# Performance work log

Hardware: AMD Instinct MI355X
Metric: run time of the kernel (lower is better)

Reference implementation:

```python
import jax, jax.numpy as jnp
import numpy as np

B, R, T, N = 64, 2, 32, 128
C_IN, C_OUT = 64, 64
PRELU_INIT = 0.25


def setup_inputs() -> dict:
    key = jax.random.key(0)
    ks = jax.random.split(key, 6)
    x = jax.random.normal(ks[0], (B, C_IN, T, N), dtype=jnp.float32)
    A = jax.random.uniform(ks[1], (B, R, T, N, N), dtype=jnp.float32)  # non-negative adjacency
    # per-relation 1x1 conv (t_kernel_size=1, relation=1 per gcn since split=[])
    w_gcn = jax.random.normal(ks[2], (R, C_OUT, C_IN), dtype=jnp.float32) * (1.0 / np.sqrt(C_IN))
    b_gcn = jnp.zeros((R, C_OUT), dtype=jnp.float32)
    # tcn temporal conv: kernel (3,1), padding (1,0)
    w_tcn = jax.random.normal(ks[3], (C_OUT, C_OUT, 3, 1), dtype=jnp.float32) * (1.0 / np.sqrt(3 * C_OUT))
    b_tcn = jnp.zeros((C_OUT,), dtype=jnp.float32)
    a_tcn = jnp.float32(PRELU_INIT)  # PReLU inside tcn
    a_out = jnp.float32(PRELU_INIT)  # final PReLU
    return {"x": x, "A": A, "w_gcn": w_gcn, "b_gcn": b_gcn,
            "w_tcn": w_tcn, "b_tcn": b_tcn, "a_tcn": a_tcn, "a_out": a_out}


def _prelu(x, a):
    return jnp.where(x >= 0, x, a * x)


def _normalized_laplacian_tilde(A):
    # A: (..., N, N); A_tilde = A + I, return D^{-1/2} A_tilde D^{-1/2}
    n = A.shape[-1]
    A_t = A + jnp.eye(n, dtype=A.dtype)
    d_inv_sqrt = jax.lax.rsqrt(A_t.sum(-1))  # (..., N); rowsum >= 1
    return d_inv_sqrt[..., :, None] * A_t * d_inv_sqrt[..., None, :]


def reference(x, A, w_gcn, b_gcn, w_tcn, b_tcn, a_tcn, a_out):
    # x: (B,C,T,N), A: (B,R,T,N,N). Eval mode: drop_edge is identity, dropout inactive.
    res = x  # in_channels == out_channels, stride == 1
    # per-relation 1x1 convs, batched over R
    x_c = jnp.einsum('bctn,roc->brotn', x, w_gcn) + b_gcn[None, :, :, None, None]
    A_norm = _normalized_laplacian_tilde(A)  # (B,R,T,N,N)
    # bmm per (r,t): out[b,c,m] = sum_n x_c[b,r,c,t,n] * A_norm[b,r,t,n,m], summed over r
    x_comb = jnp.einsum('brctn,brtnm->bctm', x_c, A_norm)
    # tcn: PReLU -> Conv2d (3,1) pad (1,0) -> Dropout(0)
    h = _prelu(x_comb, a_tcn)
    h = jax.lax.conv_general_dilated(
        h, w_tcn, window_strides=(1, 1), padding=((1, 1), (0, 0)),
        dimension_numbers=('NCHW', 'OIHW', 'NCHW'))
    h = h + b_tcn[None, :, None, None]
    out = _prelu(h + res, a_out)
    return (out, A)
```

## Files before the change

kernel.cpp:

```cpp
#include <hip/hip_runtime.h>
#include <hip/hip_bf16.h>

typedef unsigned short u16;
typedef unsigned int u32;
typedef __attribute__((ext_vector_type(8))) short bf16x8;
typedef __attribute__((ext_vector_type(4))) float f32x4;
typedef __attribute__((ext_vector_type(4))) u16 u16x4;
typedef __attribute__((ext_vector_type(8))) u16 u16x8;

#define B_ 64
#define R_ 2
#define T_ 32
#define N_ 128
#define C_ 64

__device__ __forceinline__ u16 f2bf(float f) {
  return __builtin_bit_cast(u16, __float2bfloat16(f));
}
__device__ __forceinline__ float bf2f(u16 h) {
  u32 u = ((u32)h) << 16;
  return __builtin_bit_cast(float, u);
}

#define MFMA __builtin_amdgcn_mfma_f32_16x16x32_bf16

#define BAR()                                                  \
  do {                                                         \
    asm volatile("s_waitcnt lgkmcnt(0)" ::: "memory");         \
    __builtin_amdgcn_s_barrier();                              \
    __builtin_amdgcn_sched_barrier(0);                         \
  } while (0)

__device__ __forceinline__ void a_load(float4* av, const float* Aslice, int ch, int tid) {
  const int arow = tid >> 2, aseg = tid & 3;
  const float* ap = Aslice + (size_t)(ch * 64 + arow) * N_ + aseg * 32;
#pragma unroll
  for (int j = 0; j < 8; ++j) av[j] = *(const float4*)(ap + 4 * j);
}
__device__ __forceinline__ void a_store(const float4* av, float* Oslice, int ch, int tid) {
  const int arow = tid >> 2, aseg = tid & 3;
  float* op = Oslice + (size_t)(ch * 64 + arow) * N_ + aseg * 32;
#pragma unroll
  for (int j = 0; j < 8; ++j) *(float4*)(op + 4 * j) = av[j];
}

__device__ __forceinline__ void at_write(const float4* av, int ch, int tid,
                                         u16 (*AT)[64], float* dinvr) {
  const int arow = tid >> 2, aseg = tid & 3;
  const int n = ch * 64 + arow;
  float part = 0.f;
#pragma unroll
  for (int j = 0; j < 8; ++j) part += (av[j].x + av[j].y) + (av[j].z + av[j].w);
  part += __shfl_xor(part, 1);
  part += __shfl_xor(part, 2);
  const float d = rsqrtf(part + 1.0f);
  if (aseg == 0) dinvr[n] = d;
  const int col = arow ^ (aseg << 4);
#pragma unroll
  for (int j = 0; j < 8; ++j) {
#pragma unroll
    for (int k = 0; k < 4; ++k) {
      const int m = aseg * 32 + 4 * j + k;
      float v = ((const float*)&av[j])[k];
      if (m == n) v += 1.0f;
      AT[m][col] = f2bf(v * d);
    }
  }
}

__device__ __forceinline__ void load_wg(bf16x8 wf[2][2], const float* wg, int r,
                                        int wr, int lr, int lg) {
#pragma unroll
  for (int kk = 0; kk < 2; ++kk)
#pragma unroll
    for (int mr = 0; mr < 2; ++mr) {
      const float* p = wg + ((size_t)(r * C_ + 32 * wr + 16 * mr + lr)) * C_ + 32 * kk + 8 * lg;
      float4 a = *(const float4*)p, b = *(const float4*)(p + 4);
      bf16x8 f;
      f[0] = (short)f2bf(a.x); f[1] = (short)f2bf(a.y);
      f[2] = (short)f2bf(a.z); f[3] = (short)f2bf(a.w);
      f[4] = (short)f2bf(b.x); f[5] = (short)f2bf(b.y);
      f[6] = (short)f2bf(b.z); f[7] = (short)f2bf(b.w);
      wf[kk][mr] = f;
    }
}

__device__ __forceinline__ void mm1f(u16 (*TMP)[128], const bf16x8 wf[2][2],
                                     const bf16x8 bfr[2][4], const float4 bias[2],
                                     int wr, int wc, int lr, int lg) {
  f32x4 acc1[2][4] = {};
#pragma unroll
  for (int kk = 0; kk < 2; ++kk)
#pragma unroll
    for (int mr = 0; mr < 2; ++mr)
#pragma unroll
      for (int nc = 0; nc < 4; ++nc)
        acc1[mr][nc] = MFMA(wf[kk][mr], bfr[kk][nc], acc1[mr][nc], 0, 0, 0);
#pragma unroll
  for (int mr = 0; mr < 2; ++mr) {
    const int o0 = 32 * wr + 16 * mr + 4 * lg;
    const float bb[4] = {bias[mr].x, bias[mr].y, bias[mr].z, bias[mr].w};
#pragma unroll
    for (int nc = 0; nc < 4; ++nc) {
      const int n = 64 * wc + 16 * nc + lr;
#pragma unroll
      for (int i = 0; i < 4; ++i)
        TMP[o0 + i][n ^ (i << 4)] = f2bf(acc1[mr][nc][i] + bb[i]);
    }
  }
}

__device__ __forceinline__ void mm2_half(f32x4 accr[2][4], const u16 (*TMP)[128],
                                         const u16 (*AT)[64], int ch,
                                         int wr, int wc, int lr, int lg) {
#pragma unroll
  for (int kkin = 0; kkin < 2; ++kkin) {
    bf16x8 af[2], bfr[4];
#pragma unroll
    for (int mr = 0; mr < 2; ++mr) {
      const int c = 32 * wr + 16 * mr + lr;
      const int colT = (ch * 64 + 32 * kkin + 8 * lg) ^ ((lr & 3) << 4);
      af[mr] = *(const bf16x8*)&TMP[c][colT];
    }
#pragma unroll
    for (int nc = 0; nc < 4; ++nc) {
      const int m = 64 * wc + 16 * nc + lr;
      const int colA = (32 * kkin + 8 * lg) ^ (((m >> 5) & 3) << 4);
      bfr[nc] = *(const bf16x8*)&AT[m][colA];
    }
#pragma unroll
    for (int mr = 0; mr < 2; ++mr)
#pragma unroll
      for (int nc = 0; nc < 4; ++nc)
        accr[mr][nc] = MFMA(af[mr], bfr[nc], accr[mr][nc], 0, 0, 0);
  }
}

__device__ __forceinline__ void fold(f32x4 acc2[2][4], f32x4 accr[2][4],
                                     const float* dinvr, int wc, int lr) {
#pragma unroll
  for (int nc = 0; nc < 4; ++nc) {
    const float dm = dinvr[64 * wc + 16 * nc + lr];
#pragma unroll
    for (int mr = 0; mr < 2; ++mr)
#pragma unroll
      for (int i = 0; i < 4; ++i) {
        acc2[mr][nc][i] += dm * accr[mr][nc][i];
        accr[mr][nc][i] = 0.f;
      }
  }
}

__global__ __launch_bounds__(256, 2) void k_gcn(
    const float* __restrict__ x, const float* __restrict__ A,
    const float* __restrict__ wg, const float* __restrict__ bg,
    float* __restrict__ outA, u16* __restrict__ wsX) {
  __shared__ __align__(16) u16 AT[2][N_][64];
  __shared__ __align__(16) u16 TMP[C_][128];
  __shared__ float dinv[R_][N_];

  const int tid = threadIdx.x;
  const int bid = ((blockIdx.x & 7) << 8) | (blockIdx.x >> 3);
  const int b = bid >> 5, t = bid & 31;
  const int lane = tid & 63, wv = tid >> 6;
  const int wr = wv >> 1, wc = wv & 1;
  const int lr = lane & 15, lg = lane >> 4;

  const size_t Asl0 = ((size_t)((b * R_ + 0) * T_ + t)) * (size_t)(N_ * N_);
  const size_t Asl1 = ((size_t)((b * R_ + 1) * T_ + t)) * (size_t)(N_ * N_);

  float4 xv[8];
  {
    const int c = tid & 63, ub = tid >> 6;
    const float* xp = x + ((size_t)(b * C_ + c) * T_ + t) * N_ + 32 * ub;
#pragma unroll
    for (int j = 0; j < 8; ++j) xv[j] = *(const float4*)(xp + 4 * j);
  }
  float4 avA[8], avB[8];
  a_load(avA, A + Asl0, 0, tid);
  a_load(avB, A + Asl0, 1, tid);
  bf16x8 wf0[2][2];
  load_wg(wf0, wg, 0, wr, lr, lg);
  float4 bias[R_][2];
#pragma unroll
  for (int r = 0; r < R_; ++r)
#pragma unroll
    for (int mr = 0; mr < 2; ++mr)
      bias[r][mr] = *(const float4*)(bg + r * C_ + 32 * wr + 16 * mr + 4 * lg);

  u16 (*XT)[64] = (u16(*)[64])TMP;
  {
    const int c = tid & 63, ub = tid >> 6;
#pragma unroll
    for (int j = 0; j < 8; ++j) {
      const int n0 = 32 * ub + 4 * j;
      XT[n0 + 0][c] = f2bf(xv[j].x);
      XT[n0 + 1][c ^ 16] = f2bf(xv[j].y);
      XT[n0 + 2][c ^ 32] = f2bf(xv[j].z);
      XT[n0 + 3][c ^ 48] = f2bf(xv[j].w);
    }
  }
  BAR();

  bf16x8 bfrx[2][4];
#pragma unroll
  for (int kk = 0; kk < 2; ++kk)
#pragma unroll
    for (int nc = 0; nc < 4; ++nc) {
      const int n = 64 * wc + 16 * nc + lr;
      const int col = (32 * kk + 8 * lg) ^ ((lr & 3) << 4);
      bfrx[kk][nc] = *(const bf16x8*)&XT[n][col];
    }
  BAR();

  f32x4 acc2[2][4] = {};
  f32x4 accr[2][4] = {};

  mm1f(TMP, wf0, bfrx, bias[0], wr, wc, lr, lg);
  bf16x8 wf1[2][2];
  load_wg(wf1, wg, 1, wr, lr, lg);
  at_write(avA, 0, tid, AT[0], dinv[0]);
  a_store(avA, outA + Asl0, 0, tid);
  a_load(avA, A + Asl1, 0, tid);
  BAR();

  mm2_half(accr, TMP, AT[0], 0, wr, wc, lr, lg);
  at_write(avB, 1, tid, AT[1], dinv[0]);
  a_store(avB, outA + Asl0, 1, tid);
  a_load(avB, A + Asl1, 1, tid);
  BAR();

  mm2_half(accr, TMP, AT[1], 1, wr, wc, lr, lg);
  fold(acc2, accr, dinv[0], wc, lr);
  at_write(avA, 0, tid, AT[0], dinv[1]);
  a_store(avA, outA + Asl1, 0, tid);
  BAR();

  mm1f(TMP, wf1, bfrx, bias[1], wr, wc, lr, lg);
  at_write(avB, 1, tid, AT[1], dinv[1]);
  a_store(avB, outA + Asl1, 1, tid);
  BAR();

  mm2_half(accr, TMP, AT[0], 0, wr, wc, lr, lg);
  mm2_half(accr, TMP, AT[1], 1, wr, wc, lr, lg);
  fold(acc2, accr, dinv[1], wc, lr);
  BAR();

  u16* stage = &TMP[0][0];
#pragma unroll
  for (int mr = 0; mr < 2; ++mr)
#pragma unroll
    for (int nc = 0; nc < 4; ++nc) {
      const int m = 64 * wc + 16 * nc + lr;
      const int c0 = 32 * wr + 16 * mr + 4 * lg;
#pragma unroll
      for (int i = 0; i < 4; ++i)
        stage[m * 64 + ((c0 + i) ^ ((m & 7) << 3))] = f2bf(acc2[mr][nc][i]);
    }
  BAR();
  {
    u16* wp = wsX + ((size_t)(b * T_ + t) * N_) * C_;
#pragma unroll
    for (int it = 0; it < 4; ++it) {
      const int idx = it * 2048 + tid * 8;
      const int m = idx >> 6, a = idx & 63;
      u16x8 v = *(const u16x8*)&stage[m * 64 + a];
      *(u16x8*)(wp + m * 64 + (a ^ ((m & 7) << 3))) = v;
    }
  }
}

__global__ __launch_bounds__(256, 3) void k_tcn(
    const u16* __restrict__ wsX, const float* __restrict__ x,
    const float* __restrict__ wt, const float* __restrict__ bt,
    const float* __restrict__ a_tcn, const float* __restrict__ a_out,
    float* __restrict__ out) {
  __shared__ __align__(16) u16 HT[N_][200];
  const int tid = threadIdx.x;
  const int bid = ((blockIdx.x & 7) << 8) | (blockIdx.x >> 3);
  const int b = bid >> 5, t = bid & 31;
  const int lane = tid & 63, wv = tid >> 6;
  const int wr = wv >> 1, wc = wv & 1;
  const int lr = lane & 15, lg = lane >> 4;
  const float at = a_tcn[0], ao = a_out[0];

  bf16x8 wfr[6][2];
#pragma unroll
  for (int kk = 0; kk < 6; ++kk) {
    const int dt = kk >> 1;
    const int ci0 = (32 * kk + 8 * lg) & 63;
#pragma unroll
    for (int mr = 0; mr < 2; ++mr) {
      const int co = 32 * wr + 16 * mr + lr;
      const float* p = wt + ((size_t)co * C_ + ci0) * 3 + dt;
      float e[8];
#pragma unroll
      for (int j = 0; j < 8; ++j) e[j] = p[3 * j];
      bf16x8 f;
#pragma unroll
      for (int j = 0; j < 8; ++j) f[j] = (short)f2bf(e[j]);
      wfr[kk][mr] = f;
    }
  }

#pragma unroll
  for (int dt = 0; dt < 3; ++dt) {
    const int t2 = t + dt - 1;
    const bool ok = (t2 >= 0) && (t2 < T_);
    const u16* p = wsX + ((size_t)(b * T_ + (ok ? t2 : 0)) * N_) * C_;
    u16x4 hv[8];
#pragma unroll
    for (int it = 0; it < 8; ++it) {
      const int idx = it * 256 + tid;
      const int n = idx >> 4, c4 = (idx & 15) * 4;
      u16x4 z = {0, 0, 0, 0};
      hv[it] = ok ? *(const u16x4*)(p + n * C_ + c4) : z;
    }
#pragma unroll
    for (int it = 0; it < 8; ++it) {
      const int idx = it * 256 + tid;
      const int n = idx >> 4, c4 = (idx & 15) * 4;
      u16x4 o;
#pragma unroll
      for (int j = 0; j < 4; ++j) {
        float f = bf2f(hv[it][j]);
        o[j] = f2bf(f < 0.f ? at * f : f);
      }
      *(u16x4*)&HT[n][dt * 64 + c4] = o;
    }
  }
  __syncthreads();

  f32x4 acc[2][4] = {};
#pragma unroll
  for (int kk = 0; kk < 6; ++kk) {
    bf16x8 bfr[4];
#pragma unroll
    for (int nc = 0; nc < 4; ++nc)
      bfr[nc] = *(const bf16x8*)&HT[64 * wc + 16 * nc + lr][32 * kk + 8 * lg];
#pragma unroll
    for (int mr = 0; mr < 2; ++mr)
#pragma unroll
      for (int nc = 0; nc < 4; ++nc)
        acc[mr][nc] = MFMA(wfr[kk][mr], bfr[nc], acc[mr][nc], 0, 0, 0);
  }

#pragma unroll
  for (int mr = 0; mr < 2; ++mr) {
    const int co0 = 32 * wr + 16 * mr + 4 * lg;
    float bts[4];
#pragma unroll
    for (int i = 0; i < 4; ++i) bts[i] = bt[co0 + i];
#pragma unroll
    for (int nc = 0; nc < 4; ++nc) {
      const int n = 64 * wc + 16 * nc + lr;
#pragma unroll
      for (int i = 0; i < 4; ++i) {
        const size_t gi = ((size_t)(b * C_ + co0 + i) * T_ + t) * N_ + n;
        float v = acc[mr][nc][i] + bts[i] + x[gi];
        out[gi] = (v < 0.f) ? ao * v : v;
      }
    }
  }
}

extern "C" void kernel_launch(void* const* d_in, const int* in_sizes, int n_in,
                              void* d_out, int out_size, void* d_ws, size_t ws_size,
                              hipStream_t stream) {
  const float* x = (const float*)d_in[0];
  const float* A = (const float*)d_in[1];
  const float* wg = (const float*)d_in[2];
  const float* bg = (const float*)d_in[3];
  const float* wt = (const float*)d_in[4];
  const float* bt = (const float*)d_in[5];
  const float* atc = (const float*)d_in[6];
  const float* aoc = (const float*)d_in[7];
  float* out = (float*)d_out;
  float* outA = out + (size_t)B_ * C_ * T_ * N_;
  u16* wsX = (u16*)d_ws;

  k_gcn<<<B_ * T_, 256, 0, stream>>>(x, A, wg, bg, outA, wsX);
  k_tcn<<<B_ * T_, 256, 0, stream>>>(wsX, x, wt, bt, atc, aoc, out);
}
```

Baseline: 225.6 us.

## Make k_gcn persistent over four (b,t) pairs with cross-iteration A prefetch

k_gcn now launches 512 blocks, and each block loops over four (b,t) slices. While it computes the current slice it loads the next slice's A tiles and x row into registers. The previous slice's result is staged in the AT buffer and written to the workspace at the start of the next iteration. The aim is to hide global-load latency and per-block startup behind compute. In exchange it keeps four A register buffers live, which may raise VGPR pressure or cause spills under launch_bounds(256,2).

```diff
diff --git a/kernel.cpp b/kernel.cpp
--- a/kernel.cpp
+++ b/kernel.cpp
@@ -13,6 +13,7 @@
 #define T_ 32
 #define N_ 128
 #define C_ 64
+#define NBLK 512
 
 __device__ __forceinline__ u16 f2bf(float f) {
   return __builtin_bit_cast(u16, __float2bfloat16(f));
@@ -158,113 +159,157 @@
   __shared__ __align__(16) u16 AT[2][N_][64];
   __shared__ __align__(16) u16 TMP[C_][128];
   __shared__ float dinv[R_][N_];
+  u16* stageLDS = &AT[0][0][0];
 
   const int tid = threadIdx.x;
-  const int bid = ((blockIdx.x & 7) << 8) | (blockIdx.x >> 3);
-  const int b = bid >> 5, t = bid & 31;
+  const int k0 = blockIdx.x;
+  const int kk = ((k0 & 7) << 6) | (k0 >> 3);
   const int lane = tid & 63, wv = tid >> 6;
   const int wr = wv >> 1, wc = wv & 1;
   const int lr = lane & 15, lg = lane >> 4;
 
-  const size_t Asl0 = ((size_t)((b * R_ + 0) * T_ + t)) * (size_t)(N_ * N_);
-  const size_t Asl1 = ((size_t)((b * R_ + 1) * T_ + t)) * (size_t)(N_ * N_);
+  int pair = kk;
+  size_t As0 = (size_t)(pair * R_ + 0) * (N_ * N_);
+  size_t As1 = (size_t)(pair * R_ + 1) * (N_ * N_);
+  {
+    const int b = pair >> 5, t = pair & 31;
+    As0 = ((size_t)((b * R_ + 0) * T_ + t)) * (size_t)(N_ * N_);
+    As1 = ((size_t)((b * R_ + 1) * T_ + t)) * (size_t)(N_ * N_);
+  }
 
   float4 xv[8];
   {
+    const int b = pair >> 5, t = pair & 31;
     const int c = tid & 63, ub = tid >> 6;
     const float* xp = x + ((size_t)(b * C_ + c) * T_ + t) * N_ + 32 * ub;
 #pragma unroll
     for (int j = 0; j < 8; ++j) xv[j] = *(const float4*)(xp + 4 * j);
   }
-  float4 avA[8], avB[8];
-  a_load(avA, A + Asl0, 0, tid);
-  a_load(avB, A + Asl0, 1, tid);
-  bf16x8 wf0[2][2];
-  load_wg(wf0, wg, 0, wr, lr, lg);
-  float4 bias[R_][2];
-#pragma unroll
-  for (int r = 0; r < R_; ++r)
-#pragma unroll
-    for (int mr = 0; mr < 2; ++mr)
-      bias[r][mr] = *(const float4*)(bg + r * C_ + 32 * wr + 16 * mr + 4 * lg);
-
-  u16 (*XT)[64] = (u16(*)[64])TMP;
-  {
-    const int c = tid & 63, ub = tid >> 6;
-#pragma unroll
-    for (int j = 0; j < 8; ++j) {
-      const int n0 = 32 * ub + 4 * j;
-      XT[n0 + 0][c] = f2bf(xv[j].x);
-      XT[n0 + 1][c ^ 16] = f2bf(xv[j].y);
-      XT[n0 + 2][c ^ 32] = f2bf(xv[j].z);
-      XT[n0 + 3][c ^ 48] = f2bf(xv[j].w);
-    }
-  }
-  BAR();
-
-  bf16x8 bfrx[2][4];
-#pragma unroll
-  for (int kk = 0; kk < 2; ++kk)
-#pragma unroll
-    for (int nc = 0; nc < 4; ++nc) {
-      const int n = 64 * wc + 16 * nc + lr;
-      const int col = (32 * kk + 8 * lg) ^ ((lr & 3) << 4);
-      bfrx[kk][nc] = *(const bf16x8*)&XT[n][col];
-    }
-  BAR();
+  float4 avA[8], avB[8], avC[8], avD[8];
+  a_load(avA, A + As0, 0, tid);
+  a_load(avB, A + As0, 1, tid);
+  a_load(avC, A + As1, 0, tid);
 
   f32x4 acc2[2][4] = {};
   f32x4 accr[2][4] = {};
-
-  mm1f(TMP, wf0, bfrx, bias[0], wr, wc, lr, lg);
-  bf16x8 wf1[2][2];
-  load_wg(wf1, wg, 1, wr, lr, lg);
-  at_write(avA, 0, tid, AT[0], dinv[0]);
-  a_store(avA, outA + Asl0, 0, tid);
-  a_load(avA, A + Asl1, 0, tid);
-  BAR();
-
-  mm2_half(accr, TMP, AT[0], 0, wr, wc, lr, lg);
-  at_write(avB, 1, tid, AT[1], dinv[0]);
-  a_store(avB, outA + Asl0, 1, tid);
-  a_load(avB, A + Asl1, 1, tid);
-  BAR();
-
-  mm2_half(accr, TMP, AT[1], 1, wr, wc, lr, lg);
-  fold(acc2, accr, dinv[0], wc, lr);
-  at_write(avA, 0, tid, AT[0], dinv[1]);
-  a_store(avA, outA + Asl1, 0, tid);
-  BAR();
-
-  mm1f(TMP, wf1, bfrx, bias[1], wr, wc, lr, lg);
-  at_write(avB, 1, tid, AT[1], dinv[1]);
-  a_store(avB, outA + Asl1, 1, tid);
-  BAR();
-
-  mm2_half(accr, TMP, AT[0], 0, wr, wc, lr, lg);
-  mm2_half(accr, TMP, AT[1], 1, wr, wc, lr, lg);
-  fold(acc2, accr, dinv[1], wc, lr);
-  BAR();
-
-  u16* stage = &TMP[0][0];
-#pragma unroll
-  for (int mr = 0; mr < 2; ++mr)
-#pragma unroll
-    for (int nc = 0; nc < 4; ++nc) {
-      const int m = 64 * wc + 16 * nc + lr;
-      const int c0 = 32 * wr + 16 * mr + 4 * lg;
-#pragma unroll
-      for (int i = 0; i < 4; ++i)
-        stage[m * 64 + ((c0 + i) ^ ((m & 7) << 3))] = f2bf(acc2[mr][nc][i]);
-    }
-  BAR();
+  u16 (*XT)[64] = (u16(*)[64])TMP;
+
+#pragma unroll 1
+  for (int it = 0; it < 4; ++it) {
+    const bool more = (it < 3);
+    const int npair = pair + NBLK;
+    size_t nAs0 = 0, nAs1 = 0;
+    if (more) {
+      const int nb = npair >> 5, nt = npair & 31;
+      nAs0 = ((size_t)((nb * R_ + 0) * T_ + nt)) * (size_t)(N_ * N_);
+      nAs1 = ((size_t)((nb * R_ + 1) * T_ + nt)) * (size_t)(N_ * N_);
+    }
+
+    if (it > 0) {
+      u16* wp = wsX + (size_t)(pair - NBLK) * (N_ * C_);
+#pragma unroll
+      for (int i2 = 0; i2 < 4; ++i2) {
+        const int idx = i2 * 2048 + tid * 8;
+        const int m = idx >> 6, a = idx & 63;
+        u16x8 v = *(const u16x8*)&stageLDS[m * 64 + a];
+        *(u16x8*)(wp + m * 64 + (a ^ ((m & 7) << 3))) = v;
+      }
+    }
+    {
+      const int c = tid & 63, ub = tid >> 6;
+#pragma unroll
+      for (int j = 0; j < 8; ++j) {
+        const int n0 = 32 * ub + 4 * j;
+        XT[n0 + 0][c] = f2bf(xv[j].x);
+        XT[n0 + 1][c ^ 16] = f2bf(xv[j].y);
+        XT[n0 + 2][c ^ 32] = f2bf(xv[j].z);
+        XT[n0 + 3][c ^ 48] = f2bf(xv[j].w);
+      }
+    }
+    BAR();
+
+    bf16x8 bfrx[2][4];
+#pragma unroll
+    for (int kq = 0; kq < 2; ++kq)
+#pragma unroll
+      for (int nc = 0; nc < 4; ++nc) {
+        const int n = 64 * wc + 16 * nc + lr;
+        const int col = (32 * kq + 8 * lg) ^ ((lr & 3) << 4);
+        bfrx[kq][nc] = *(const bf16x8*)&XT[n][col];
+      }
+    bf16x8 wf0[2][2];
+    load_wg(wf0, wg, 0, wr, lr, lg);
+    float4 bias[R_][2];
+#pragma unroll
+    for (int r = 0; r < R_; ++r)
+#pragma unroll
+      for (int mr = 0; mr < 2; ++mr)
+        bias[r][mr] = *(const float4*)(bg + r * C_ + 32 * wr + 16 * mr + 4 * lg);
+    BAR();
+
+    mm1f(TMP, wf0, bfrx, bias[0], wr, wc, lr, lg);
+    at_write(avA, 0, tid, AT[0], dinv[0]);
+    a_store(avA, outA + As0, 0, tid);
+    a_load(avD, A + As1, 1, tid);
+    BAR();
+
+    mm2_half(accr, TMP, AT[0], 0, wr, wc, lr, lg);
+    at_write(avB, 1, tid, AT[1], dinv[0]);
+    a_store(avB, outA + As0, 1, tid);
+    if (more) a_load(avA, A + nAs0, 0, tid);
+    bf16x8 wf1[2][2];
+    load_wg(wf1, wg, 1, wr, lr, lg);
+    BAR();
+
+    mm2_half(accr, TMP, AT[1], 1, wr, wc, lr, lg);
+    fold(acc2, accr, dinv[0], wc, lr);
+    at_write(avC, 0, tid, AT[0], dinv[1]);
+    a_store(avC, outA + As1, 0, tid);
+    if (more) a_load(avB, A + nAs0, 1, tid);
+    BAR();
+
+    mm1f(TMP, wf1, bfrx, bias[1], wr, wc, lr, lg);
+    at_write(avD, 1, tid, AT[1], dinv[1]);
+    a_store(avD, outA + As1, 1, tid);
+    if (more) a_load(avC, A + nAs1, 0, tid);
+    BAR();
+
+    mm2_half(accr, TMP, AT[0], 0, wr, wc, lr, lg);
+    mm2_half(accr, TMP, AT[1], 1, wr, wc, lr, lg);
+    fold(acc2, accr, dinv[1], wc, lr);
+    if (more) {
+      const int nb = npair >> 5, nt = npair & 31;
+      const int c = tid & 63, ub = tid >> 6;
+      const float* xp = x + ((size_t)(nb * C_ + c) * T_ + nt) * N_ + 32 * ub;
+#pragma unroll
+      for (int j = 0; j < 8; ++j) xv[j] = *(const float4*)(xp + 4 * j);
+    }
+    BAR();
+
+#pragma unroll
+    for (int mr = 0; mr < 2; ++mr)
+#pragma unroll
+      for (int nc = 0; nc < 4; ++nc) {
+        const int m = 64 * wc + 16 * nc + lr;
+        const int c0 = 32 * wr + 16 * mr + 4 * lg;
+#pragma unroll
+        for (int i = 0; i < 4; ++i) {
+          stageLDS[m * 64 + ((c0 + i) ^ ((m & 7) << 3))] = f2bf(acc2[mr][nc][i]);
+          acc2[mr][nc][i] = 0.f;
+        }
+      }
+    BAR();
+
+    if (more) { pair = npair; As0 = nAs0; As1 = nAs1; }
+  }
+
   {
-    u16* wp = wsX + ((size_t)(b * T_ + t) * N_) * C_;
-#pragma unroll
-    for (int it = 0; it < 4; ++it) {
-      const int idx = it * 2048 + tid * 8;
+    u16* wp = wsX + (size_t)pair * (N_ * C_);
+#pragma unroll
+    for (int i2 = 0; i2 < 4; ++i2) {
+      const int idx = i2 * 2048 + tid * 8;
       const int m = idx >> 6, a = idx & 63;
-      u16x8 v = *(const u16x8*)&stage[m * 64 + a];
+      u16x8 v = *(const u16x8*)&stageLDS[m * 64 + a];
       *(u16x8*)(wp + m * 64 + (a ^ ((m & 7) << 3))) = v;
     }
   }
@@ -286,9 +331,9 @@
 
   bf16x8 wfr[6][2];
 #pragma unroll
-  for (int kk = 0; kk < 6; ++kk) {
-    const int dt = kk >> 1;
-    const int ci0 = (32 * kk + 8 * lg) & 63;
+  for (int kq = 0; kq < 6; ++kq) {
+    const int dt = kq >> 1;
+    const int ci0 = (32 * kq + 8 * lg) & 63;
 #pragma unroll
     for (int mr = 0; mr < 2; ++mr) {
       const int co = 32 * wr + 16 * mr + lr;
@@ -299,7 +344,7 @@
       bf16x8 f;
 #pragma unroll
       for (int j = 0; j < 8; ++j) f[j] = (short)f2bf(e[j]);
-      wfr[kk][mr] = f;
+      wfr[kq][mr] = f;
     }
   }
 
@@ -310,20 +355,20 @@
     const u16* p = wsX + ((size_t)(b * T_ + (ok ? t2 : 0)) * N_) * C_;
     u16x4 hv[8];
 #pragma unroll
-    for (int it = 0; it < 8; ++it) {
-      const int idx = it * 256 + tid;
+    for (int i3 = 0; i3 < 8; ++i3) {
+      const int idx = i3 * 256 + tid;
       const int n = idx >> 4, c4 = (idx & 15) * 4;
       u16x4 z = {0, 0, 0, 0};
-      hv[it] = ok ? *(const u16x4*)(p + n * C_ + c4) : z;
-    }
-#pragma unroll
-    for (int it = 0; it < 8; ++it) {
-      const int idx = it * 256 + tid;
+      hv[i3] = ok ? *(const u16x4*)(p + n * C_ + c4) : z;
+    }
+#pragma unroll
+    for (int i3 = 0; i3 < 8; ++i3) {
+      const int idx = i3 * 256 + tid;
       const int n = idx >> 4, c4 = (idx & 15) * 4;
       u16x4 o;
 #pragma unroll
       for (int j = 0; j < 4; ++j) {
-        float f = bf2f(hv[it][j]);
+        float f = bf2f(hv[i3][j]);
         o[j] = f2bf(f < 0.f ? at * f : f);
       }
       *(u16x4*)&HT[n][dt * 64 + c4] = o;
@@ -333,16 +378,16 @@
 
   f32x4 acc[2][4] = {};
 #pragma unroll
-  for (int kk = 0; kk < 6; ++kk) {
+  for (int kq = 0; kq < 6; ++kq) {
     bf16x8 bfr[4];
 #pragma unroll
     for (int nc = 0; nc < 4; ++nc)
-      bfr[nc] = *(const bf16x8*)&HT[64 * wc + 16 * nc + lr][32 * kk + 8 * lg];
+      bfr[nc] = *(const bf16x8*)&HT[64 * wc + 16 * nc + lr][32 * kq + 8 * lg];
 #pragma unroll
     for (int mr = 0; mr < 2; ++mr)
 #pragma unroll
       for (int nc = 0; nc < 4; ++nc)
-        acc[mr][nc] = MFMA(wfr[kk][mr], bfr[nc], acc[mr][nc], 0, 0, 0);
+        acc[mr][nc] = MFMA(wfr[kq][mr], bfr[nc], acc[mr][nc], 0, 0, 0);
   }
 
 #pragma unroll
@@ -379,6 +424,6 @@
   float* outA = out + (size_t)B_ * C_ * T_ * N_;
   u16* wsX = (u16*)d_ws;
 
-  k_gcn<<<B_ * T_, 256, 0, stream>>>(x, A, wg, bg, outA, wsX);
+  k_gcn<<<NBLK, 256, 0, stream>>>(x, A, wg, bg, outA, wsX);
   k_tcn<<<B_ * T_, 256, 0, stream>>>(wsX, x, wt, bt, atc, aoc, out);
 }
```

Measured after the change: 324.7 us. +44.0%, slower.
